# Performance work log

Measured on AMD Instinct MI355X. Metric: run time of the kernel, lower is better.

Reference implementation:

```python
import jax, jax.numpy as jnp
import numpy as np

# init config (from module __init__ / docstring example)
VOXEL_SIZE = np.array([0.2, 0.2, 8.0], dtype=np.float32)
PC_RANGE = np.array([0.0, -25.6, -3.0, 51.2, 25.6, 5.0], dtype=np.float32)
MAX_PTS = 32
MAX_VOX = 16000
GRID = (int((PC_RANGE[3] - PC_RANGE[0]) / VOXEL_SIZE[0]),
        int((PC_RANGE[4] - PC_RANGE[1]) / VOXEL_SIZE[1]),
        int((PC_RANGE[5] - PC_RANGE[2]) / VOXEL_SIZE[2]))  # (256, 256, 1)

N_POINTS = 4_000_000
C_FEAT = 4  # xyz + intensity


def setup_inputs() -> dict:
    key = jax.random.key(0)
    u = jax.random.uniform(key, (N_POINTS, C_FEAT), dtype=jnp.float32)
    lo = jnp.array([PC_RANGE[0], PC_RANGE[1], PC_RANGE[2], 0.0], jnp.float32)
    span = jnp.array([PC_RANGE[3] - PC_RANGE[0], PC_RANGE[4] - PC_RANGE[1],
                      PC_RANGE[5] - PC_RANGE[2], 1.0], jnp.float32)
    points = u * span + lo  # uniformly inside the point-cloud range
    return {"points": points}


def reference(points):
    """Hard voxelization. Returns fixed-size (padded) outputs:
    voxels [MAX_VOX, MAX_PTS, C], coords [MAX_VOX, 3] int32, num_points [MAX_VOX] int32.
    Unused voxel slots are zero (num_points==0), matching torch semantics up to padding."""
    N, C = points.shape
    Gx, Gy, Gz = GRID
    lo = jnp.asarray(PC_RANGE[:3])
    hi = jnp.asarray(PC_RANGE[3:])
    vsz = jnp.asarray(VOXEL_SIZE)

    xyz = points[:, :3]
    valid = jnp.all((xyz >= lo) & (xyz < hi), axis=1)  # in-range mask

    coords = jnp.floor((xyz - lo) / vsz).astype(jnp.int32)
    coords = jnp.clip(coords, 0, jnp.array([Gx - 1, Gy - 1, Gz - 1], jnp.int32))

    # linear voxel hash; invalid points get sentinel so they sort to the end
    BIG = Gx * Gy * Gz
    vhash = coords[:, 0] * (Gy * Gz) + coords[:, 1] * Gz + coords[:, 2]
    vhash = jnp.where(valid, vhash, BIG)

    order = jnp.argsort(vhash)
    sh = vhash[order]          # [N] sorted hashes
    sc = coords[order]         # [N,3]
    sp = points[order]         # [N,C]
    svalid = sh < BIG

    # segment boundaries of the sorted hash stream (== torch.unique inverse groups)
    newv = jnp.concatenate([jnp.array([True]), sh[1:] != sh[:-1]]) & svalid
    vid = jnp.cumsum(newv.astype(jnp.int32)) - 1   # voxel id per point (sorted order)

    idx = jnp.arange(N, dtype=jnp.int32)
    start = jax.lax.cummax(jnp.where(newv, idx, 0))  # index of first point of own voxel
    rank = idx - start                                # position within voxel

    keep = svalid & (rank < MAX_PTS) & (vid < MAX_VOX)
    vid_s = jnp.where(keep, vid, MAX_VOX)   # route dropped points to dump row
    rank_s = jnp.where(keep, rank, 0)

    voxels = jnp.zeros((MAX_VOX + 1, MAX_PTS, C), points.dtype)
    voxels = voxels.at[vid_s, rank_s].set(sp)[:MAX_VOX]

    cvid = jnp.where(newv & (vid < MAX_VOX), vid, MAX_VOX)
    coords_out = jnp.zeros((MAX_VOX + 1, 3), jnp.int32).at[cvid].set(sc)[:MAX_VOX]

    num_points = jax.ops.segment_sum(keep.astype(jnp.int32), vid_s,
                                     num_segments=MAX_VOX + 1)[:MAX_VOX]
    return voxels, coords_out, num_points
```

## Files before the change

kernel.cpp:

```cpp
#include <hip/hip_runtime.h>

#define NBINS    65536
#define NWORDS   16384
#define MAXVOX   16000
#define MAXPTS   32
#define NBLK     256
#define RSEG     8

#define COORDS_OFF (MAXVOX * MAXPTS * 4)
#define NP_OFF     (COORDS_OFF + MAXVOX * 3)

#define OFF_COUNTS   0u
#define OFF_STARTS   (256u << 10)
#define OFF_BINOF    (512u << 10)
#define OFF_PARTC    (576u << 10)
#define OFF_PARTO    (577u << 10)
#define OFF_BINS     (1u << 20)
#define OFF_PARTIAL  (17u << 20)
#define OFF_MEMBERS  (33u << 20)

__global__ __launch_bounds__(1024) void k_hist(const float4* __restrict__ pts, int n,
                                               unsigned* __restrict__ bins,
                                               unsigned* __restrict__ partial) {
    __shared__ unsigned sh[NWORDS];
    int t = threadIdx.x, b = blockIdx.x;
    for (int w = t; w < NWORDS; w += 1024) sh[w] = 0u;
    __syncthreads();

    int chunk = (n + NBLK - 1) / NBLK;
    int s = b * chunk;
    int e = min(n, s + chunk);
    for (int i = s + t; i < e; i += 1024) {
        float4 p = pts[i];
        bool valid = (p.x >= 0.0f)   & (p.x < 51.2f) &
                     (p.y >= -25.6f) & (p.y < 25.6f) &
                     (p.z >= -3.0f)  & (p.z < 5.0f);
        int cx = (int)floorf((p.x - 0.0f)  / 0.2f);
        int cy = (int)floorf((p.y + 25.6f) / 0.2f);
        int cz = (int)floorf((p.z + 3.0f)  / 8.0f);
        cx = min(max(cx, 0), 255);
        cy = min(max(cy, 0), 255);
        cz = min(max(cz, 0), 0);
        unsigned bin = (unsigned)(cx * 256 + cy + cz);
        if (valid) {
            bins[i] = bin;
            atomicAdd(&sh[bin >> 2], 1u << ((bin & 3u) * 8u));
        } else {
            bins[i] = 0xFFFFFFFFu;
        }
    }
    __syncthreads();
    unsigned* myp = partial + (size_t)b * NWORDS;
    for (int w = t; w < NWORDS; w += 1024) myp[w] = sh[w];
}

__global__ __launch_bounds__(512) void k_reduce(unsigned* __restrict__ partial,
                                                unsigned* __restrict__ counts,
                                                unsigned* __restrict__ partC,
                                                unsigned* __restrict__ partO,
                                                unsigned* __restrict__ binof) {
    __shared__ unsigned segsum[RSEG][64][4];
    __shared__ unsigned red[512];
    int t = threadIdx.x;
    int g = blockIdx.x * 512 + t;
    if (g < MAXVOX) binof[g] = 0xFFFFFFFFu;

    int wl  = t & 63;
    int seg = t >> 6;
    int w   = blockIdx.x * 64 + wl;
    int blk0 = seg * (NBLK / RSEG);

    unsigned a0 = 0, a1 = 0, a2 = 0, a3 = 0;
    for (int b = 0; b < NBLK / RSEG; ++b) {
        unsigned v = partial[(size_t)(blk0 + b) * NWORDS + w];
        a0 += v & 255u; a1 += (v >> 8) & 255u;
        a2 += (v >> 16) & 255u; a3 += (v >> 24) & 255u;
    }
    segsum[seg][wl][0] = a0; segsum[seg][wl][1] = a1;
    segsum[seg][wl][2] = a2; segsum[seg][wl][3] = a3;
    __syncthreads();

    unsigned b0 = 0, b1 = 0, b2 = 0, b3 = 0;
    for (int s2 = 0; s2 < seg; ++s2) {
        b0 += segsum[s2][wl][0]; b1 += segsum[s2][wl][1];
        b2 += segsum[s2][wl][2]; b3 += segsum[s2][wl][3];
    }
    for (int b = 0; b < NBLK / RSEG; ++b) {
        size_t idx = (size_t)(blk0 + b) * NWORDS + w;
        unsigned v = partial[idx];
        partial[idx] = b0 | (b1 << 8) | (b2 << 16) | (b3 << 24);
        b0 += v & 255u; b1 += (v >> 8) & 255u;
        b2 += (v >> 16) & 255u; b3 += (v >> 24) & 255u;
    }

    unsigned mySum = 0, myOcc = 0;
    if (seg == RSEG - 1) {
        counts[w * 4 + 0] = b0; counts[w * 4 + 1] = b1;
        counts[w * 4 + 2] = b2; counts[w * 4 + 3] = b3;
        mySum = b0 + b1 + b2 + b3;
        myOcc = (b0 > 0u) + (b1 > 0u) + (b2 > 0u) + (b3 > 0u);
    }
    red[t] = mySum; __syncthreads();
    for (int off = 256; off > 0; off >>= 1) { if (t < off) red[t] += red[t + off]; __syncthreads(); }
    if (t == 0) partC[blockIdx.x] = red[0];
    __syncthreads();
    red[t] = myOcc; __syncthreads();
    for (int off = 256; off > 0; off >>= 1) { if (t < off) red[t] += red[t + off]; __syncthreads(); }
    if (t == 0) partO[blockIdx.x] = red[0];
}

__global__ __launch_bounds__(256) void k_scan3(const unsigned* __restrict__ counts,
                                               const unsigned* __restrict__ partC,
                                               const unsigned* __restrict__ partO,
                                               unsigned* __restrict__ starts,
                                               unsigned* __restrict__ binof,
                                               float* __restrict__ out) {
    __shared__ unsigned rc[256], ro[256], sc[256], so[256];
    int t = threadIdx.x;
    int bin = blockIdx.x * 256 + t;
    unsigned c = counts[bin];
    unsigned occ = (c > 0u) ? 1u : 0u;

    rc[t] = (t < blockIdx.x) ? partC[t] : 0u;
    ro[t] = (t < blockIdx.x) ? partO[t] : 0u;
    sc[t] = c; so[t] = occ;
    __syncthreads();
    for (int off = 128; off > 0; off >>= 1) {
        if (t < off) { rc[t] += rc[t + off]; ro[t] += ro[t + off]; }
        __syncthreads();
    }
    unsigned baseC = rc[0], baseO = ro[0];
    for (int off = 1; off < 256; off <<= 1) {
        unsigned ac = (t >= off) ? sc[t - off] : 0u;
        unsigned ao = (t >= off) ? so[t - off] : 0u;
        __syncthreads();
        sc[t] += ac; so[t] += ao;
        __syncthreads();
    }
    unsigned st  = baseC + (sc[t] - c);
    unsigned vid = baseO + (so[t] - occ);
    bool kept = occ && (vid < MAXVOX);
    starts[bin] = st | (kept ? 0u : 0x80000000u);
    if (kept) {
        binof[vid] = (unsigned)bin;
        out[COORDS_OFF + vid * 3 + 0] = (float)(bin >> 8);
        out[COORDS_OFF + vid * 3 + 1] = (float)(bin & 255);
        out[COORDS_OFF + vid * 3 + 2] = 0.0f;
        out[NP_OFF + vid] = (float)(c < MAXPTS ? c : MAXPTS);
    }
}

__global__ __launch_bounds__(1024) void k_scatter(const unsigned* __restrict__ bins, int n,
                                                  const unsigned* __restrict__ partial,
                                                  const unsigned* __restrict__ starts,
                                                  unsigned* __restrict__ members) {
    __shared__ unsigned sh[NWORDS];
    int t = threadIdx.x, b = blockIdx.x;
    const unsigned* myp = partial + (size_t)b * NWORDS;
    for (int w = t; w < NWORDS; w += 1024) sh[w] = myp[w];
    __syncthreads();

    int chunk = (n + NBLK - 1) / NBLK;
    int s = b * chunk;
    int e = min(n, s + chunk);
    for (int i = s + t; i < e; i += 1024) {
        unsigned v = bins[i];
        if (v == 0xFFFFFFFFu) continue;
        unsigned st = starts[v];
        if (st & 0x80000000u) continue;
        unsigned old = atomicAdd(&sh[v >> 2], 1u << ((v & 3u) * 8u));
        unsigned off = (old >> ((v & 3u) * 8u)) & 255u;
        members[st + off] = (unsigned)i;
    }
}

__global__ __launch_bounds__(256) void k_select(
        const unsigned* __restrict__ binof, const unsigned* __restrict__ counts,
        const unsigned* __restrict__ starts, const unsigned* __restrict__ members,
        const float4* __restrict__ pts, float* __restrict__ out) {
    float4* vox = (float4*)out;
    int v = blockIdx.x * 4 + (threadIdx.x >> 6);
    unsigned lane = threadIdx.x & 63u;
    const float4 z4 = {0.0f, 0.0f, 0.0f, 0.0f};
    unsigned bin = binof[v];
    if (bin == 0xFFFFFFFFu) {
        if (lane < 32u) vox[(size_t)v * MAXPTS + lane] = z4;
        if (lane < 3u)  out[COORDS_OFF + v * 3 + lane] = 0.0f;
        if (lane == 3u) out[NP_OFF + v] = 0.0f;
        return;
    }
    unsigned m  = counts[bin];
    unsigned mc = m > 256u ? 256u : m;
    unsigned np = m > 32u ? 32u : m;
    unsigned start = starts[bin] & 0x7FFFFFFFu;

    if (lane >= np && lane < 32u) vox[(size_t)v * MAXPTS + lane] = z4;

    if (mc <= 64u) {
        unsigned e0 = (lane < mc) ? members[start + lane] : 0xFFFFFFFFu;
        unsigned r0 = 0;
        int jm = (int)mc;
        for (int j = 0; j < jm; ++j) {
            unsigned a0 = (unsigned)__shfl((int)e0, j);
            r0 += (a0 < e0);
        }
        if (e0 != 0xFFFFFFFFu && r0 < MAXPTS) vox[(size_t)v * MAXPTS + r0] = pts[e0];
    } else if (mc <= 128u) {
        unsigned e0 = members[start + lane];
        unsigned e1 = (lane + 64u < mc) ? members[start + lane + 64u] : 0xFFFFFFFFu;
        unsigned r0 = 0, r1 = 0;
        for (int j = 0; j < 64; ++j) {
            unsigned a0 = (unsigned)__shfl((int)e0, j);
            unsigned a1 = (unsigned)__shfl((int)e1, j);
            r0 += (a0 < e0) + (a1 < e0);
            r1 += (a0 < e1) + (a1 < e1);
        }
        if (r0 < MAXPTS) vox[(size_t)v * MAXPTS + r0] = pts[e0];
        if (e1 != 0xFFFFFFFFu && r1 < MAXPTS) vox[(size_t)v * MAXPTS + r1] = pts[e1];
    } else {
        unsigned e0 = members[start + lane];
        unsigned e1 = members[start + lane + 64u];
        unsigned e2 = (lane + 128u < mc) ? members[start + lane + 128u] : 0xFFFFFFFFu;
        unsigned e3 = (lane + 192u < mc) ? members[start + lane + 192u] : 0xFFFFFFFFu;
        unsigned r0 = 0, r1 = 0, r2 = 0, r3 = 0;
        for (int j = 0; j < 64; ++j) {
            unsigned a0 = (unsigned)__shfl((int)e0, j);
            unsigned a1 = (unsigned)__shfl((int)e1, j);
            unsigned a2 = (unsigned)__shfl((int)e2, j);
            unsigned a3 = (unsigned)__shfl((int)e3, j);
            r0 += (a0 < e0) + (a1 < e0) + (a2 < e0) + (a3 < e0);
            r1 += (a0 < e1) + (a1 < e1) + (a2 < e1) + (a3 < e1);
            r2 += (a0 < e2) + (a1 < e2) + (a2 < e2) + (a3 < e2);
            r3 += (a0 < e3) + (a1 < e3) + (a2 < e3) + (a3 < e3);
        }
        if (r0 < MAXPTS) vox[(size_t)v * MAXPTS + r0] = pts[e0];
        if (r1 < MAXPTS) vox[(size_t)v * MAXPTS + r1] = pts[e1];
        if (e2 != 0xFFFFFFFFu && r2 < MAXPTS) vox[(size_t)v * MAXPTS + r2] = pts[e2];
        if (e3 != 0xFFFFFFFFu && r3 < MAXPTS) vox[(size_t)v * MAXPTS + r3] = pts[e3];
    }
}

extern "C" void kernel_launch(void* const* d_in, const int* in_sizes, int n_in,
                              void* d_out, int out_size, void* d_ws, size_t ws_size,
                              hipStream_t stream) {
    const float4* pts = (const float4*)d_in[0];
    int n = in_sizes[0] / 4;
    float* out = (float*)d_out;
    char* ws = (char*)d_ws;

    unsigned* counts  = (unsigned*)(ws + OFF_COUNTS);
    unsigned* starts  = (unsigned*)(ws + OFF_STARTS);
    unsigned* binof   = (unsigned*)(ws + OFF_BINOF);
    unsigned* partC   = (unsigned*)(ws + OFF_PARTC);
    unsigned* partO   = (unsigned*)(ws + OFF_PARTO);
    unsigned* bins    = (unsigned*)(ws + OFF_BINS);
    unsigned* partial = (unsigned*)(ws + OFF_PARTIAL);
    unsigned* members = (unsigned*)(ws + OFF_MEMBERS);

    k_hist   <<<NBLK, 1024, 0, stream>>>(pts, n, bins, partial);
    k_reduce <<<NWORDS / 64, 512, 0, stream>>>(partial, counts, partC, partO, binof);
    k_scan3  <<<256, 256, 0, stream>>>(counts, partC, partO, starts, binof, out);
    k_scatter<<<NBLK, 1024, 0, stream>>>(bins, n, partial, starts, members);
    k_select <<<MAXVOX / 4, 256, 0, stream>>>(binof, counts, starts, members, pts, out);
}
```

Before: 76.81 us.

## Compress per-point bins to 16-bit with ballot validity bitmask; cache partials in LDS

```diff
diff --git a/kernel.cpp b/kernel.cpp
--- a/kernel.cpp
+++ b/kernel.cpp
@@ -15,12 +15,14 @@
 #define OFF_BINOF    (512u << 10)
 #define OFF_PARTC    (576u << 10)
 #define OFF_PARTO    (577u << 10)
-#define OFF_BINS     (1u << 20)
-#define OFF_PARTIAL  (17u << 20)
-#define OFF_MEMBERS  (33u << 20)
+#define OFF_VBIT     (640u << 10)
+#define OFF_BINS16   (2u << 20)
+#define OFF_PARTIAL  (10u << 20)
+#define OFF_MEMBERS  (26u << 20)
 
 __global__ __launch_bounds__(1024) void k_hist(const float4* __restrict__ pts, int n,
-                                               unsigned* __restrict__ bins,
+                                               unsigned short* __restrict__ bins16,
+                                               unsigned long long* __restrict__ vbit,
                                                unsigned* __restrict__ partial) {
     __shared__ unsigned sh[NWORDS];
     int t = threadIdx.x, b = blockIdx.x;
@@ -30,7 +32,8 @@
     int chunk = (n + NBLK - 1) / NBLK;
     int s = b * chunk;
     int e = min(n, s + chunk);
-    for (int i = s + t; i < e; i += 1024) {
+    int k = 0;
+    for (int i = s + t; i < e; i += 1024, ++k) {
         float4 p = pts[i];
         bool valid = (p.x >= 0.0f)   & (p.x < 51.2f) &
                      (p.y >= -25.6f) & (p.y < 25.6f) &
@@ -42,12 +45,10 @@
         cy = min(max(cy, 0), 255);
         cz = min(max(cz, 0), 0);
         unsigned bin = (unsigned)(cx * 256 + cy + cz);
-        if (valid) {
-            bins[i] = bin;
-            atomicAdd(&sh[bin >> 2], 1u << ((bin & 3u) * 8u));
-        } else {
-            bins[i] = 0xFFFFFFFFu;
-        }
+        bins16[i] = (unsigned short)bin;
+        unsigned long long mask = __ballot(valid);
+        if ((t & 63) == 0) vbit[(size_t)b * 256 + (t >> 6) + k * 16] = mask;
+        if (valid) atomicAdd(&sh[bin >> 2], 1u << ((bin & 3u) * 8u));
     }
     __syncthreads();
     unsigned* myp = partial + (size_t)b * NWORDS;
@@ -59,6 +60,7 @@
                                                 unsigned* __restrict__ partC,
                                                 unsigned* __restrict__ partO,
                                                 unsigned* __restrict__ binof) {
+    __shared__ unsigned cache[NBLK][64];
     __shared__ unsigned segsum[RSEG][64][4];
     __shared__ unsigned red[512];
     int t = threadIdx.x;
@@ -73,6 +75,7 @@
     unsigned a0 = 0, a1 = 0, a2 = 0, a3 = 0;
     for (int b = 0; b < NBLK / RSEG; ++b) {
         unsigned v = partial[(size_t)(blk0 + b) * NWORDS + w];
+        cache[blk0 + b][wl] = v;
         a0 += v & 255u; a1 += (v >> 8) & 255u;
         a2 += (v >> 16) & 255u; a3 += (v >> 24) & 255u;
     }
@@ -86,9 +89,9 @@
         b2 += segsum[s2][wl][2]; b3 += segsum[s2][wl][3];
     }
     for (int b = 0; b < NBLK / RSEG; ++b) {
-        size_t idx = (size_t)(blk0 + b) * NWORDS + w;
-        unsigned v = partial[idx];
-        partial[idx] = b0 | (b1 << 8) | (b2 << 16) | (b3 << 24);
+        unsigned v = cache[blk0 + b][wl];
+        partial[(size_t)(blk0 + b) * NWORDS + w] =
+            b0 | (b1 << 8) | (b2 << 16) | (b3 << 24);
         b0 += v & 255u; b1 += (v >> 8) & 255u;
         b2 += (v >> 16) & 255u; b3 += (v >> 24) & 255u;
     }
@@ -150,7 +153,9 @@
     }
 }
 
-__global__ __launch_bounds__(1024) void k_scatter(const unsigned* __restrict__ bins, int n,
+__global__ __launch_bounds__(1024) void k_scatter(const unsigned short* __restrict__ bins16,
+                                                  const unsigned long long* __restrict__ vbit,
+                                                  int n,
                                                   const unsigned* __restrict__ partial,
                                                   const unsigned* __restrict__ starts,
                                                   unsigned* __restrict__ members) {
@@ -163,14 +168,18 @@
     int chunk = (n + NBLK - 1) / NBLK;
     int s = b * chunk;
     int e = min(n, s + chunk);
-    for (int i = s + t; i < e; i += 1024) {
-        unsigned v = bins[i];
-        if (v == 0xFFFFFFFFu) continue;
-        unsigned st = starts[v];
-        if (st & 0x80000000u) continue;
-        unsigned old = atomicAdd(&sh[v >> 2], 1u << ((v & 3u) * 8u));
-        unsigned off = (old >> ((v & 3u) * 8u)) & 255u;
-        members[st + off] = (unsigned)i;
+    int k = 0;
+    for (int i = s + t; i < e; i += 1024, ++k) {
+        unsigned long long mask = vbit[(size_t)b * 256 + (t >> 6) + k * 16];
+        if ((mask >> (t & 63)) & 1ull) {
+            unsigned v = (unsigned)bins16[i];
+            unsigned st = starts[v];
+            if (!(st & 0x80000000u)) {
+                unsigned old = atomicAdd(&sh[v >> 2], 1u << ((v & 3u) * 8u));
+                unsigned off = (old >> ((v & 3u) * 8u)) & 255u;
+                members[st + off] = (unsigned)i;
+            }
+        }
     }
 }
 
@@ -253,13 +262,14 @@
     unsigned* binof   = (unsigned*)(ws + OFF_BINOF);
     unsigned* partC   = (unsigned*)(ws + OFF_PARTC);
     unsigned* partO   = (unsigned*)(ws + OFF_PARTO);
-    unsigned* bins    = (unsigned*)(ws + OFF_BINS);
+    unsigned long long* vbit = (unsigned long long*)(ws + OFF_VBIT);
+    unsigned short* bins16   = (unsigned short*)(ws + OFF_BINS16);
     unsigned* partial = (unsigned*)(ws + OFF_PARTIAL);
     unsigned* members = (unsigned*)(ws + OFF_MEMBERS);
 
-    k_hist   <<<NBLK, 1024, 0, stream>>>(pts, n, bins, partial);
+    k_hist   <<<NBLK, 1024, 0, stream>>>(pts, n, bins16, vbit, partial);
     k_reduce <<<NWORDS / 64, 512, 0, stream>>>(partial, counts, partC, partO, binof);
     k_scan3  <<<256, 256, 0, stream>>>(counts, partC, partO, starts, binof, out);
-    k_scatter<<<NBLK, 1024, 0, stream>>>(bins, n, partial, starts, members);
+    k_scatter<<<NBLK, 1024, 0, stream>>>(bins16, vbit, n, partial, starts, members);
     k_select <<<MAXVOX / 4, 256, 0, stream>>>(binof, counts, starts, members, pts, out);
 }
```

Result: no change. 77.02 us (+0.3%).
